# Kernel tuning notes

Hardware: AMD Instinct MI355X
Metric: run time of the kernel (lower is better)

Reference implementation:

```python
import jax, jax.numpy as jnp
import numpy as np

DM = 1024
NH = 16  # matches init_kwargs nh


def setup_inputs() -> dict:
    key = jax.random.key(0)
    ks = jax.random.split(key, 9)
    B, S = 8, 1024
    sc = 1.0 / np.sqrt(DM)
    return {
        "x": jax.random.normal(ks[0], (B, S, DM), jnp.float32),
        "Wq": jax.random.normal(ks[1], (DM, DM), jnp.float32) * sc,
        "bq": jax.random.normal(ks[2], (DM,), jnp.float32) * 0.02,
        "Wk": jax.random.normal(ks[3], (DM, DM), jnp.float32) * sc,
        "bk": jax.random.normal(ks[4], (DM,), jnp.float32) * 0.02,
        "Wv": jax.random.normal(ks[5], (DM, DM), jnp.float32) * sc,
        "bv": jax.random.normal(ks[6], (DM,), jnp.float32) * 0.02,
        "Wo": jax.random.normal(ks[7], (DM, DM), jnp.float32) * sc,
        "bo": jax.random.normal(ks[8], (DM,), jnp.float32) * 0.02,
    }


def reference(x, Wq, bq, Wk, bk, Wv, bv, Wo, bo):
    B, S, dm = x.shape
    H = NH
    dk = dm // H
    # torch nn.Linear: y = x @ W.T + b
    Q = (x @ Wq.T + bq).reshape(B, S, H, dk)
    K = (x @ Wk.T + bk).reshape(B, S, H, dk)
    V = (x @ Wv.T + bv).reshape(B, S, H, dk)
    # per-head scores q @ k^T, NO 1/sqrt(dk) scaling (faithful to source)
    scores = jnp.einsum('bqhd,bkhd->hbqk', Q, K)  # [H, B, S, S]
    # torch.softmax(..., dim=0) on a [B, S, S] tensor -> softmax over BATCH axis
    attn = jax.nn.softmax(scores, axis=1)
    heads = jnp.einsum('hbqk,bkhd->bqhd', attn, V).reshape(B, S, dm)
    return heads @ Wo.T + bo
```

## Files before the change

kernel.cpp:

```cpp
#include <hip/hip_runtime.h>
#include <hip/hip_bf16.h>

#define DM 1024
#define NH 16
#define DK 64
#define BB 8
#define SS 1024
#define MROWS (BB * SS)

typedef _Float16 f16;
using f32x4 = __attribute__((ext_vector_type(4))) float;
using f16x8 = __attribute__((ext_vector_type(8))) _Float16;
using f16x4 = __attribute__((ext_vector_type(4))) _Float16;

using lds_ptr_t = __attribute__((address_space(3))) void*;
using glb_ptr_t = const __attribute__((address_space(1))) void*;

__device__ __forceinline__ void glds16(const void* g, void* l) {
  __builtin_amdgcn_global_load_lds((glb_ptr_t)g, (lds_ptr_t)l, 16, 0, 0);
}

__global__ __launch_bounds__(256) void cast_kernel(const float* __restrict__ src,
                                                   f16* __restrict__ dst,
                                                   int n) {
  int i = (blockIdx.x * 256 + threadIdx.x) * 4;
  if (i < n) {
    float4 v = *reinterpret_cast<const float4*>(src + i);
    f16x4 o;
    o[0] = (f16)v.x; o[1] = (f16)v.y; o[2] = (f16)v.z; o[3] = (f16)v.w;
    *reinterpret_cast<f16x4*>(dst + i) = o;
  }
}

template <int MODE>
__global__ __launch_bounds__(256) void gemm_bt(const f16* __restrict__ A,
                                               const f16* __restrict__ Bm,
                                               const float* __restrict__ bias,
                                               void* __restrict__ Out) {
  __shared__ f16 As[128 * 32];
  __shared__ f16 Bs[128 * 32];
  const int t = threadIdx.x;
  const int lane = t & 63;
  const int w = t >> 6;
  const int wm = w >> 1, wn = w & 1;
  const int bm = blockIdx.x * 128;
  const int bn = blockIdx.y * 128;
  const int l15 = lane & 15;
  const int g = lane >> 4;

  const f16* a0 = A + (size_t)bm * DM;
  const f16* b0 = Bm + (size_t)bn * DM;

  f32x4 acc[4][4] = {};

  const int c0 = w * 64 + lane;
  const int c1 = 256 + w * 64 + lane;

  for (int kt = 0; kt < DM / 32; ++kt) {
    const int k0 = kt * 32;
    glds16(a0 + (size_t)(c0 >> 2) * DM + k0 + (c0 & 3) * 8, As + (size_t)(w * 64) * 8);
    glds16(a0 + (size_t)(c1 >> 2) * DM + k0 + (c1 & 3) * 8, As + (size_t)(256 + w * 64) * 8);
    glds16(b0 + (size_t)(c0 >> 2) * DM + k0 + (c0 & 3) * 8, Bs + (size_t)(w * 64) * 8);
    glds16(b0 + (size_t)(c1 >> 2) * DM + k0 + (c1 & 3) * 8, Bs + (size_t)(256 + w * 64) * 8);
    __syncthreads();

    f16x8 af[4], bfr[4];
#pragma unroll
    for (int m = 0; m < 4; ++m)
      af[m] = *(const f16x8*)(As + (wm * 64 + m * 16 + l15) * 32 + g * 8);
#pragma unroll
    for (int n = 0; n < 4; ++n)
      bfr[n] = *(const f16x8*)(Bs + (wn * 64 + n * 16 + l15) * 32 + g * 8);
#pragma unroll
    for (int m = 0; m < 4; ++m)
#pragma unroll
      for (int n = 0; n < 4; ++n)
        acc[m][n] = __builtin_amdgcn_mfma_f32_16x16x32_f16(af[m], bfr[n], acc[m][n], 0, 0, 0);
    __syncthreads();
  }

#pragma unroll
  for (int n = 0; n < 4; ++n) {
    const int j = bn + wn * 64 + n * 16 + l15;
    const float bj = bias[j];
#pragma unroll
    for (int m = 0; m < 4; ++m) {
      const int ib = bm + wm * 64 + m * 16 + g * 4;
#pragma unroll
      for (int r = 0; r < 4; ++r) {
        const int i = ib + r;
        const float val = acc[m][n][r] + bj;
        if (MODE == 0) {
          const int b = i >> 10, s = i & 1023, h = j >> 6, d = j & 63;
          ((f16*)Out)[((size_t)((b * 16 + h) * 1024 + s)) * 64 + d] = (f16)val;
        } else if (MODE == 1) {
          const int b = i >> 10, s = i & 1023, h = j >> 6, d = j & 63;
          ((f16*)Out)[((size_t)((b * 16 + h) * 64 + d)) * 1024 + s] = (f16)val;
        } else {
          ((float*)Out)[(size_t)i * DM + j] = val;
        }
      }
    }
  }
}

#define PS 1057

__global__ __launch_bounds__(512) void attn_kernel(const f16* __restrict__ Qr,
                                                   const f16* __restrict__ Kr,
                                                   const f16* __restrict__ Vt,
                                                   f16* __restrict__ Hd) {
  __shared__ float Sx[8 * PS];
  __shared__ float Dinv[32 * 33];

  const int t = threadIdx.x;
  const int lane = t & 63;
  const int b = t >> 6;
  const int h = blockIdx.y;
  const int qt = blockIdx.x;
  const int l15 = lane & 15;
  const int g = lane >> 4;

  const size_t plane = ((size_t)(b * 16 + h) * 1024) * 64;
  const f16* Qp = Qr + plane;
  const f16* Kp = Kr + plane;
  const f16* Vp = Vt + ((size_t)(b * 16 + h) * 64) * 1024;

  f16x8 qf[2][2];
#pragma unroll
  for (int i = 0; i < 2; ++i)
#pragma unroll
    for (int db = 0; db < 2; ++db)
      qf[i][db] = *(const f16x8*)(Qp + (size_t)(qt * 32 + i * 16 + l15) * 64 + db * 32 + g * 8);

  f32x4 oacc[2][4] = {};

  for (int kt = 0; kt < 32; ++kt) {
    f32x4 sacc[2][2] = {};
#pragma unroll
    for (int kf = 0; kf < 2; ++kf)
#pragma unroll
      for (int db = 0; db < 2; ++db) {
        f16x8 kfr = *(const f16x8*)(Kp + (size_t)(kt * 32 + kf * 16 + l15) * 64 + db * 32 + g * 8);
#pragma unroll
        for (int i = 0; i < 2; ++i)
          sacc[i][kf] = __builtin_amdgcn_mfma_f32_16x16x32_f16(qf[i][db], kfr, sacc[i][kf], 0, 0, 0);
      }
#pragma unroll
    for (int i = 0; i < 2; ++i)
#pragma unroll
      for (int kf = 0; kf < 2; ++kf)
#pragma unroll
        for (int r = 0; r < 4; ++r) {
          float e = __expf(sacc[i][kf][r]);
          Sx[b * PS + (i * 16 + g * 4 + r) * 33 + kf * 16 + l15] = e;
        }
    __syncthreads();
#pragma unroll
    for (int pp = 0; pp < 2; ++pp) {
      const int p = t + pp * 512;
      const int q = p >> 5, k = p & 31;
      float sden = 0.f;
#pragma unroll
      for (int bb2 = 0; bb2 < 8; ++bb2) sden += Sx[bb2 * PS + q * 33 + k];
      Dinv[q * 33 + k] = __builtin_amdgcn_rcpf(sden);
    }
    __syncthreads();
    f16x8 pf[2];
#pragma unroll
    for (int i = 0; i < 2; ++i) {
      const int row = i * 16 + l15;
      union { f16x8 v; f16 hh[8]; } u;
#pragma unroll
      for (int j = 0; j < 8; ++j) {
        const int k = g * 8 + j;
        u.hh[j] = (f16)(Sx[b * PS + row * 33 + k] * Dinv[row * 33 + k]);
      }
      pf[i] = u.v;
    }
#pragma unroll
    for (int n = 0; n < 4; ++n) {
      f16x8 vf = *(const f16x8*)(Vp + (size_t)(n * 16 + l15) * 1024 + kt * 32 + g * 8);
#pragma unroll
      for (int i = 0; i < 2; ++i)
        oacc[i][n] = __builtin_amdgcn_mfma_f32_16x16x32_f16(pf[i], vf, oacc[i][n], 0, 0, 0);
    }
    __syncthreads();
  }

#pragma unroll
  for (int i = 0; i < 2; ++i)
#pragma unroll
    for (int n = 0; n < 4; ++n)
#pragma unroll
      for (int r = 0; r < 4; ++r) {
        const int srow = qt * 32 + i * 16 + g * 4 + r;
        const int d = n * 16 + l15;
        Hd[((size_t)(b * 1024 + srow)) * 1024 + h * 64 + d] = (f16)oacc[i][n][r];
      }
}

extern "C" void kernel_launch(void* const* d_in, const int* in_sizes, int n_in,
                              void* d_out, int out_size, void* d_ws, size_t ws_size,
                              hipStream_t stream) {
  const float* x  = (const float*)d_in[0];
  const float* Wq = (const float*)d_in[1];
  const float* bq = (const float*)d_in[2];
  const float* Wk = (const float*)d_in[3];
  const float* bk = (const float*)d_in[4];
  const float* Wv = (const float*)d_in[5];
  const float* bv = (const float*)d_in[6];
  const float* Wo = (const float*)d_in[7];
  const float* bo = (const float*)d_in[8];

  char* ws = (char*)d_ws;
  const size_t MB = 1u << 20;
  f16* xf  = (f16*)(ws + 0 * MB);
  f16* Wqf = (f16*)(ws + 16 * MB);
  f16* Wkf = (f16*)(ws + 18 * MB);
  f16* Wvf = (f16*)(ws + 20 * MB);
  f16* Wof = (f16*)(ws + 22 * MB);
  f16* Qr  = (f16*)(ws + 24 * MB);
  f16* Kr  = (f16*)(ws + 40 * MB);
  f16* Vt  = (f16*)(ws + 56 * MB);
  f16* Hd  = xf;

  cast_kernel<<<8192, 256, 0, stream>>>(x, xf, MROWS * DM);
  cast_kernel<<<1024, 256, 0, stream>>>(Wq, Wqf, DM * DM);
  cast_kernel<<<1024, 256, 0, stream>>>(Wk, Wkf, DM * DM);
  cast_kernel<<<1024, 256, 0, stream>>>(Wv, Wvf, DM * DM);
  cast_kernel<<<1024, 256, 0, stream>>>(Wo, Wof, DM * DM);

  dim3 gg(MROWS / 128, DM / 128);
  gemm_bt<0><<<gg, 256, 0, stream>>>(xf, Wqf, bq, (void*)Qr);
  gemm_bt<0><<<gg, 256, 0, stream>>>(xf, Wkf, bk, (void*)Kr);
  gemm_bt<1><<<gg, 256, 0, stream>>>(xf, Wvf, bv, (void*)Vt);

  attn_kernel<<<dim3(SS / 32, NH), 512, 0, stream>>>(Qr, Kr, Vt, Hd);

  gemm_bt<2><<<gg, 256, 0, stream>>>(Hd, Wof, bo, d_out);
}
```

Before: 336.6 us.

## Batch weight casts and QKV GEMMs, restructure attention with LDS atomic denominators

The four weight casts become one launch, and the three QKV projections become a single grid with a z dimension, which cuts launch count and improves occupancy. The attention kernel now keeps the exponentials in registers and accumulates the cross-batch denominators with LDS atomics, double-buffered over pairs of key tiles, instead of staging the full score tile through shared memory. Probabilities go through a small per-wave f16 scratch. The kernel also adds setprio around the MFMAs, an XCD-aware block remap and a launch_bounds occupancy hint. The risks are LDS atomic contention and the extra register pressure from holding the exponentials.

```diff
diff --git a/kernel.cpp b/kernel.cpp
--- a/kernel.cpp
+++ b/kernel.cpp
@@ -3,7 +3,6 @@
 
 #define DM 1024
 #define NH 16
-#define DK 64
 #define BB 8
 #define SS 1024
 #define MROWS (BB * SS)
@@ -12,6 +11,7 @@
 using f32x4 = __attribute__((ext_vector_type(4))) float;
 using f16x8 = __attribute__((ext_vector_type(8))) _Float16;
 using f16x4 = __attribute__((ext_vector_type(4))) _Float16;
+using hf16x2 = __attribute__((ext_vector_type(2))) __fp16;
 
 using lds_ptr_t = __attribute__((address_space(3))) void*;
 using glb_ptr_t = const __attribute__((address_space(1))) void*;
@@ -32,11 +32,101 @@
   }
 }
 
-template <int MODE>
-__global__ __launch_bounds__(256) void gemm_bt(const f16* __restrict__ A,
-                                               const f16* __restrict__ Bm,
-                                               const float* __restrict__ bias,
-                                               void* __restrict__ Out) {
+struct WC {
+  const float *s0, *s1, *s2, *s3;
+  f16 *d0, *d1, *d2, *d3;
+};
+__global__ __launch_bounds__(256) void wcast_kernel(WC a) {
+  const int seg = blockIdx.x >> 10;
+  const int blk = blockIdx.x & 1023;
+  const float* s = (seg == 0) ? a.s0 : (seg == 1) ? a.s1 : (seg == 2) ? a.s2 : a.s3;
+  f16* d = (seg == 0) ? a.d0 : (seg == 1) ? a.d1 : (seg == 2) ? a.d2 : a.d3;
+  const int i = (blk * 256 + threadIdx.x) * 4;
+  float4 v = *reinterpret_cast<const float4*>(s + i);
+  f16x4 o;
+  o[0] = (f16)v.x; o[1] = (f16)v.y; o[2] = (f16)v.z; o[3] = (f16)v.w;
+  *reinterpret_cast<f16x4*>(d + i) = o;
+}
+
+struct QKVArgs {
+  const f16 *A, *B0, *B1, *B2;
+  const float *bi0, *bi1, *bi2;
+  f16 *O0, *O1, *O2;
+};
+__global__ __launch_bounds__(256) void qkv_gemm(QKVArgs p) {
+  __shared__ f16 As[128 * 32];
+  __shared__ f16 Bs[128 * 32];
+  const int t = threadIdx.x;
+  const int lane = t & 63;
+  const int w = t >> 6;
+  const int wm = w >> 1, wn = w & 1;
+  const int bm = blockIdx.x * 128;
+  const int bn = blockIdx.y * 128;
+  const int z = blockIdx.z;
+  const int l15 = lane & 15;
+  const int g = lane >> 4;
+
+  const f16* Bmat = (z == 0) ? p.B0 : (z == 1) ? p.B1 : p.B2;
+  const float* bias = (z == 0) ? p.bi0 : (z == 1) ? p.bi1 : p.bi2;
+
+  const f16* a0 = p.A + (size_t)bm * DM;
+  const f16* b0 = Bmat + (size_t)bn * DM;
+
+  f32x4 acc[4][4] = {};
+
+  const int c0 = w * 64 + lane;
+  const int c1 = 256 + w * 64 + lane;
+
+  for (int kt = 0; kt < DM / 32; ++kt) {
+    const int k0 = kt * 32;
+    glds16(a0 + (size_t)(c0 >> 2) * DM + k0 + (c0 & 3) * 8, As + (size_t)(w * 64) * 8);
+    glds16(a0 + (size_t)(c1 >> 2) * DM + k0 + (c1 & 3) * 8, As + (size_t)(256 + w * 64) * 8);
+    glds16(b0 + (size_t)(c0 >> 2) * DM + k0 + (c0 & 3) * 8, Bs + (size_t)(w * 64) * 8);
+    glds16(b0 + (size_t)(c1 >> 2) * DM + k0 + (c1 & 3) * 8, Bs + (size_t)(256 + w * 64) * 8);
+    __syncthreads();
+
+    f16x8 af[4], bfr[4];
+#pragma unroll
+    for (int m = 0; m < 4; ++m)
+      af[m] = *(const f16x8*)(As + (wm * 64 + m * 16 + l15) * 32 + g * 8);
+#pragma unroll
+    for (int n = 0; n < 4; ++n)
+      bfr[n] = *(const f16x8*)(Bs + (wn * 64 + n * 16 + l15) * 32 + g * 8);
+#pragma unroll
+    for (int m = 0; m < 4; ++m)
+#pragma unroll
+      for (int n = 0; n < 4; ++n)
+        acc[m][n] = __builtin_amdgcn_mfma_f32_16x16x32_f16(af[m], bfr[n], acc[m][n], 0, 0, 0);
+    __syncthreads();
+  }
+
+  f16* Out = (z == 0) ? p.O0 : (z == 1) ? p.O1 : p.O2;
+#pragma unroll
+  for (int n = 0; n < 4; ++n) {
+    const int j = bn + wn * 64 + n * 16 + l15;
+    const float bj = bias[j];
+#pragma unroll
+    for (int m = 0; m < 4; ++m) {
+      const int ib = bm + wm * 64 + m * 16 + g * 4;
+#pragma unroll
+      for (int r = 0; r < 4; ++r) {
+        const int i = ib + r;
+        const float val = acc[m][n][r] + bj;
+        const int b = i >> 10, s = i & 1023, h = j >> 6, d = j & 63;
+        if (z < 2) {
+          Out[((size_t)((b * 16 + h) * 1024 + s)) * 64 + d] = (f16)val;
+        } else {
+          Out[((size_t)((b * 16 + h) * 64 + d)) * 1024 + s] = (f16)val;
+        }
+      }
+    }
+  }
+}
+
+__global__ __launch_bounds__(256) void gemm_out(const f16* __restrict__ A,
+                                                const f16* __restrict__ Bm,
+                                                const float* __restrict__ bias,
+                                                float* __restrict__ Out) {
   __shared__ f16 As[128 * 32];
   __shared__ f16 Bs[128 * 32];
   const int t = threadIdx.x;
@@ -89,114 +179,131 @@
 #pragma unroll
       for (int r = 0; r < 4; ++r) {
         const int i = ib + r;
-        const float val = acc[m][n][r] + bj;
-        if (MODE == 0) {
-          const int b = i >> 10, s = i & 1023, h = j >> 6, d = j & 63;
-          ((f16*)Out)[((size_t)((b * 16 + h) * 1024 + s)) * 64 + d] = (f16)val;
-        } else if (MODE == 1) {
-          const int b = i >> 10, s = i & 1023, h = j >> 6, d = j & 63;
-          ((f16*)Out)[((size_t)((b * 16 + h) * 64 + d)) * 1024 + s] = (f16)val;
-        } else {
-          ((float*)Out)[(size_t)i * DM + j] = val;
-        }
-      }
-    }
-  }
-}
-
-#define PS 1057
-
-__global__ __launch_bounds__(512) void attn_kernel(const f16* __restrict__ Qr,
-                                                   const f16* __restrict__ Kr,
-                                                   const f16* __restrict__ Vt,
-                                                   f16* __restrict__ Hd) {
-  __shared__ float Sx[8 * PS];
-  __shared__ float Dinv[32 * 33];
+        Out[(size_t)i * DM + j] = acc[m][n][r] + bj;
+      }
+    }
+  }
+}
+
+#define DSTR 67
+#define PSTR 40
+
+__global__ __launch_bounds__(512, 4) void attn_kernel(const f16* __restrict__ Qr,
+                                                      const f16* __restrict__ Kr,
+                                                      const f16* __restrict__ Vt,
+                                                      f16* __restrict__ Hd) {
+  __shared__ float Dsum[2][32 * DSTR];
+  __shared__ unsigned short Pscr[8][32 * PSTR];
 
   const int t = threadIdx.x;
   const int lane = t & 63;
   const int b = t >> 6;
-  const int h = blockIdx.y;
-  const int qt = blockIdx.x;
   const int l15 = lane & 15;
   const int g = lane >> 4;
 
-  const size_t plane = ((size_t)(b * 16 + h) * 1024) * 64;
+  const int bid = blockIdx.x;
+  const int L = (bid & 7) * 64 + (bid >> 3);
+  const int h = L >> 5;
+  const int qt = L & 31;
+
+  const size_t plane = (size_t)(b * NH + h) * SS * 64;
   const f16* Qp = Qr + plane;
   const f16* Kp = Kr + plane;
-  const f16* Vp = Vt + ((size_t)(b * 16 + h) * 64) * 1024;
-
-  f16x8 qf[2][2];
-#pragma unroll
-  for (int i = 0; i < 2; ++i)
+  const f16* Vp = Vt + (size_t)(b * NH + h) * 64 * SS;
+
+  f16x8 qfr[2][2];
+#pragma unroll
+  for (int qf = 0; qf < 2; ++qf)
 #pragma unroll
     for (int db = 0; db < 2; ++db)
-      qf[i][db] = *(const f16x8*)(Qp + (size_t)(qt * 32 + i * 16 + l15) * 64 + db * 32 + g * 8);
+      qfr[qf][db] = *(const f16x8*)(Qp + (size_t)(qt * 32 + qf * 16 + l15) * 64 + db * 32 + g * 8);
+
+  for (int p = t; p < 32 * DSTR; p += 512) Dsum[0][p] = 0.f;
+  __syncthreads();
 
   f32x4 oacc[2][4] = {};
-
-  for (int kt = 0; kt < 32; ++kt) {
-    f32x4 sacc[2][2] = {};
-#pragma unroll
-    for (int kf = 0; kf < 2; ++kf)
+  float e[2][2][2][4];
+
+  for (int grp = 0; grp < 16; ++grp) {
+    const int cur = grp & 1, nxt = cur ^ 1;
+#pragma unroll
+    for (int t2 = 0; t2 < 2; ++t2) {
+      const int kt = grp * 2 + t2;
+      f32x4 sacc[2][2] = {};
 #pragma unroll
       for (int db = 0; db < 2; ++db) {
-        f16x8 kfr = *(const f16x8*)(Kp + (size_t)(kt * 32 + kf * 16 + l15) * 64 + db * 32 + g * 8);
-#pragma unroll
-        for (int i = 0; i < 2; ++i)
-          sacc[i][kf] = __builtin_amdgcn_mfma_f32_16x16x32_f16(qf[i][db], kfr, sacc[i][kf], 0, 0, 0);
-      }
-#pragma unroll
-    for (int i = 0; i < 2; ++i)
+        f16x8 k0 = *(const f16x8*)(Kp + (size_t)(kt * 32 + 0 * 16 + l15) * 64 + db * 32 + g * 8);
+        f16x8 k1 = *(const f16x8*)(Kp + (size_t)(kt * 32 + 1 * 16 + l15) * 64 + db * 32 + g * 8);
+        __builtin_amdgcn_s_setprio(1);
+#pragma unroll
+        for (int qf = 0; qf < 2; ++qf) {
+          sacc[0][qf] = __builtin_amdgcn_mfma_f32_16x16x32_f16(k0, qfr[qf][db], sacc[0][qf], 0, 0, 0);
+          sacc[1][qf] = __builtin_amdgcn_mfma_f32_16x16x32_f16(k1, qfr[qf][db], sacc[1][qf], 0, 0, 0);
+        }
+        __builtin_amdgcn_s_setprio(0);
+      }
 #pragma unroll
       for (int kf = 0; kf < 2; ++kf)
 #pragma unroll
-        for (int r = 0; r < 4; ++r) {
-          float e = __expf(sacc[i][kf][r]);
-          Sx[b * PS + (i * 16 + g * 4 + r) * 33 + kf * 16 + l15] = e;
+        for (int qf = 0; qf < 2; ++qf)
+#pragma unroll
+          for (int r = 0; r < 4; ++r) {
+            const float ev = __expf(sacc[kf][qf][r]);
+            e[t2][kf][qf][r] = ev;
+            atomicAdd(&Dsum[cur][(qf * 16 + l15) * DSTR + t2 * 32 + kf * 16 + g * 4 + r], ev);
+          }
+    }
+    __syncthreads();
+    for (int p = t; p < 2048; p += 512) {
+      const int idx = (p >> 6) * DSTR + (p & 63);
+      Dsum[cur][idx] = __builtin_amdgcn_rcpf(Dsum[cur][idx]);
+      Dsum[nxt][idx] = 0.f;
+    }
+    __syncthreads();
+#pragma unroll
+    for (int t2 = 0; t2 < 2; ++t2) {
+      const int kt = grp * 2 + t2;
+#pragma unroll
+      for (int kf = 0; kf < 2; ++kf)
+#pragma unroll
+        for (int qf = 0; qf < 2; ++qf) {
+          const int dbase = (qf * 16 + l15) * DSTR + t2 * 32 + kf * 16 + g * 4;
+          const float p0 = e[t2][kf][qf][0] * Dsum[cur][dbase + 0];
+          const float p1 = e[t2][kf][qf][1] * Dsum[cur][dbase + 1];
+          const float p2 = e[t2][kf][qf][2] * Dsum[cur][dbase + 2];
+          const float p3 = e[t2][kf][qf][3] * Dsum[cur][dbase + 3];
+          union { hf16x2 h; unsigned u; } ulo, uhi;
+          ulo.h = __builtin_amdgcn_cvt_pkrtz(p0, p1);
+          uhi.h = __builtin_amdgcn_cvt_pkrtz(p2, p3);
+          uint2 wv; wv.x = ulo.u; wv.y = uhi.u;
+          *reinterpret_cast<uint2*>(&Pscr[b][(qf * 16 + l15) * PSTR + kf * 16 + g * 4]) = wv;
         }
-    __syncthreads();
-#pragma unroll
-    for (int pp = 0; pp < 2; ++pp) {
-      const int p = t + pp * 512;
-      const int q = p >> 5, k = p & 31;
-      float sden = 0.f;
-#pragma unroll
-      for (int bb2 = 0; bb2 < 8; ++bb2) sden += Sx[bb2 * PS + q * 33 + k];
-      Dinv[q * 33 + k] = __builtin_amdgcn_rcpf(sden);
-    }
-    __syncthreads();
-    f16x8 pf[2];
-#pragma unroll
-    for (int i = 0; i < 2; ++i) {
-      const int row = i * 16 + l15;
-      union { f16x8 v; f16 hh[8]; } u;
-#pragma unroll
-      for (int j = 0; j < 8; ++j) {
-        const int k = g * 8 + j;
-        u.hh[j] = (f16)(Sx[b * PS + row * 33 + k] * Dinv[row * 33 + k]);
-      }
-      pf[i] = u.v;
-    }
-#pragma unroll
-    for (int n = 0; n < 4; ++n) {
-      f16x8 vf = *(const f16x8*)(Vp + (size_t)(n * 16 + l15) * 1024 + kt * 32 + g * 8);
-#pragma unroll
-      for (int i = 0; i < 2; ++i)
-        oacc[i][n] = __builtin_amdgcn_mfma_f32_16x16x32_f16(pf[i], vf, oacc[i][n], 0, 0, 0);
-    }
-    __syncthreads();
-  }
-
-#pragma unroll
-  for (int i = 0; i < 2; ++i)
-#pragma unroll
-    for (int n = 0; n < 4; ++n)
+      asm volatile("" ::: "memory");
+      f16x8 pf[2];
+#pragma unroll
+      for (int qf = 0; qf < 2; ++qf)
+        pf[qf] = *(const f16x8*)&Pscr[b][(qf * 16 + l15) * PSTR + g * 8];
+      __builtin_amdgcn_s_setprio(1);
+#pragma unroll
+      for (int nf = 0; nf < 4; ++nf) {
+        f16x8 vf = *(const f16x8*)(Vp + (size_t)(nf * 16 + l15) * SS + kt * 32 + g * 8);
+#pragma unroll
+        for (int qf = 0; qf < 2; ++qf)
+          oacc[qf][nf] = __builtin_amdgcn_mfma_f32_16x16x32_f16(pf[qf], vf, oacc[qf][nf], 0, 0, 0);
+      }
+      __builtin_amdgcn_s_setprio(0);
+    }
+  }
+
+#pragma unroll
+  for (int qf = 0; qf < 2; ++qf)
+#pragma unroll
+    for (int nf = 0; nf < 4; ++nf)
 #pragma unroll
       for (int r = 0; r < 4; ++r) {
-        const int srow = qt * 32 + i * 16 + g * 4 + r;
-        const int d = n * 16 + l15;
-        Hd[((size_t)(b * 1024 + srow)) * 1024 + h * 64 + d] = (f16)oacc[i][n][r];
+        const int srow = qt * 32 + qf * 16 + g * 4 + r;
+        const int d = nf * 16 + l15;
+        Hd[((size_t)(b * 1024 + srow)) * 1024 + h * 64 + d] = (f16)oacc[qf][nf][r];
       }
 }
 
@@ -226,17 +333,13 @@
   f16* Hd  = xf;
 
   cast_kernel<<<8192, 256, 0, stream>>>(x, xf, MROWS * DM);
-  cast_kernel<<<1024, 256, 0, stream>>>(Wq, Wqf, DM * DM);
-  cast_kernel<<<1024, 256, 0, stream>>>(Wk, Wkf, DM * DM);
-  cast_kernel<<<1024, 256, 0, stream>>>(Wv, Wvf, DM * DM);
-  cast_kernel<<<1024, 256, 0, stream>>>(Wo, Wof, DM * DM);
-
-  dim3 gg(MROWS / 128, DM / 128);
-  gemm_bt<0><<<gg, 256, 0, stream>>>(xf, Wqf, bq, (void*)Qr);
-  gemm_bt<0><<<gg, 256, 0, stream>>>(xf, Wkf, bk, (void*)Kr);
-  gemm_bt<1><<<gg, 256, 0, stream>>>(xf, Wvf, bv, (void*)Vt);
-
-  attn_kernel<<<dim3(SS / 32, NH), 512, 0, stream>>>(Qr, Kr, Vt, Hd);
-
-  gemm_bt<2><<<gg, 256, 0, stream>>>(Hd, Wof, bo, d_out);
-}
+  WC wc{Wq, Wk, Wv, Wo, Wqf, Wkf, Wvf, Wof};
+  wcast_kernel<<<4096, 256, 0, stream>>>(wc);
+
+  QKVArgs qa{xf, Wqf, Wkf, Wvf, bq, bk, bv, Qr, Kr, Vt};
+  qkv_gemm<<<dim3(MROWS / 128, DM / 128, 3), 256, 0, stream>>>(qa);
+
+  attn_kernel<<<512, 512, 0, stream>>>(Qr, Kr, Vt, Hd);
+
+  gemm_out<<<dim3(MROWS / 128, DM / 128), 256, 0, stream>>>(Hd, Wof, bo, (float*)d_out);
+}
```

Result: slower. 938.2 us (+178.7%).
